# Kernel tuning notes

Hardware: AMD Instinct MI355X
Metric: run time of the kernel (lower is better)

## Reference

```python
import jax, jax.numpy as jnp
import numpy as np

NUM_EMBEDDINGS = 8192
EMBEDDING_DIM = 256
PROJECTION_DIM = 128


def setup_inputs() -> dict:
    key = jax.random.key(0)
    k_x, k_cb, k_w, k_b = jax.random.split(key, 4)
    x = jax.random.normal(k_x, (16, 1024, EMBEDDING_DIM), dtype=jnp.float32)
    codebook = jax.random.normal(k_cb, (NUM_EMBEDDINGS, EMBEDDING_DIM), dtype=jnp.float32)
    proj_w = jax.random.normal(k_w, (EMBEDDING_DIM, PROJECTION_DIM), dtype=jnp.float32) / np.sqrt(EMBEDDING_DIM)
    proj_b = jax.random.normal(k_b, (PROJECTION_DIM,), dtype=jnp.float32) * 0.01
    return {"x": x, "codebook": codebook, "proj_w": proj_w, "proj_b": proj_b}


def reference(x, codebook, proj_w, proj_b):
    # Flatten tokens: [N, D]
    x_flat = x.reshape(-1, EMBEDDING_DIM)
    # Project tokens and codebook into the distance space: [N, P], [K, P]
    x_proj = x_flat @ proj_w + proj_b
    cb_proj = codebook @ proj_w + proj_b
    # Squared euclidean distances via expansion: [N, K]
    distances = (
        jnp.sum(x_proj ** 2, axis=1, keepdims=True)
        - 2.0 * (x_proj @ cb_proj.T)
        + jnp.sum(cb_proj ** 2, axis=1)
    )
    idx = jnp.argmin(distances, axis=1)
    discrete = jax.nn.one_hot(idx, NUM_EMBEDDINGS, dtype=x.dtype)  # [N, K]
    # One-hot matmul lookup (disguised gather): [N, D]
    quantized = (discrete @ codebook).reshape(x.shape)
    return (discrete, quantized)
```

## Files before the change

kernel.cpp:

```cpp
#include <hip/hip_runtime.h>
#include <math.h>

#define D 256
#define P 128
#define K 8192
#define NTOK 16384
#define NROWS (NTOK + K)
#define CAPC 64
#define MARGIN 3.0f
#define FLT_BIG 3.402823466e+38f

typedef __attribute__((ext_vector_type(8))) short bf16x8;
typedef __attribute__((ext_vector_type(4))) float f32x4;
typedef __attribute__((ext_vector_type(8))) unsigned short u16x8;

__device__ __forceinline__ unsigned short f32_to_bf16_rne(float f) {
    unsigned int u = __float_as_uint(f);
    u = (u + 0x7fffu + ((u >> 16) & 1u)) >> 16;
    return (unsigned short)u;
}

__global__ __launch_bounds__(256) void proj_kernel(
    const float* __restrict__ x, const float* __restrict__ cb,
    const float* __restrict__ w, const float* __restrict__ bias,
    float* __restrict__ xproj, float* __restrict__ cproj,
    float* __restrict__ xnorm, float* __restrict__ cnorm,
    unsigned short* __restrict__ xh, unsigned short* __restrict__ chs,
    int* __restrict__ cnt, int* __restrict__ gmin)
{
    __shared__ float As[16][D];
    const int tid = threadIdx.x;
    const int row0 = blockIdx.x * 16;

    {
        int g = blockIdx.x * 256 + tid;
        if (g < NTOK) { cnt[g] = 0; gmin[g] = 0x7F7FFFFF; }
    }

    for (int i = tid; i < 16 * (D / 4); i += 256) {
        int r = i / (D / 4);
        int c4 = i % (D / 4);
        int gr = row0 + r;
        const float* src = (gr < NTOK) ? (x + (size_t)gr * D)
                                       : (cb + (size_t)(gr - NTOK) * D);
        float4 v = ((const float4*)src)[c4];
        ((float4*)&As[r][0])[c4] = v;
    }
    __syncthreads();

    const int r = tid >> 4;
    const int c0 = (tid & 15) * 8;

    float acc[8];
#pragma unroll
    for (int j = 0; j < 8; j++) acc[j] = 0.f;

    for (int d = 0; d < D; d += 4) {
        float4 a4 = *(const float4*)&As[r][d];
#pragma unroll
        for (int dd = 0; dd < 4; dd++) {
            float av = (dd == 0) ? a4.x : (dd == 1) ? a4.y : (dd == 2) ? a4.z : a4.w;
            float4 w0 = *(const float4*)&w[(size_t)(d + dd) * P + c0];
            float4 w1 = *(const float4*)&w[(size_t)(d + dd) * P + c0 + 4];
            acc[0] = fmaf(av, w0.x, acc[0]);
            acc[1] = fmaf(av, w0.y, acc[1]);
            acc[2] = fmaf(av, w0.z, acc[2]);
            acc[3] = fmaf(av, w0.w, acc[3]);
            acc[4] = fmaf(av, w1.x, acc[4]);
            acc[5] = fmaf(av, w1.y, acc[5]);
            acc[6] = fmaf(av, w1.z, acc[6]);
            acc[7] = fmaf(av, w1.w, acc[7]);
        }
    }

    float out[8];
    float nrm = 0.f;
    u16x8 hv;
#pragma unroll
    for (int j = 0; j < 8; j++) {
        out[j] = acc[j] + bias[c0 + j];
        nrm = fmaf(out[j], out[j], nrm);
        hv[j] = f32_to_bf16_rne(out[j]);
    }

    const int gr = row0 + r;
    float4 o0; o0.x = out[0]; o0.y = out[1]; o0.z = out[2]; o0.w = out[3];
    float4 o1; o1.x = out[4]; o1.y = out[5]; o1.z = out[6]; o1.w = out[7];
    if (gr < NTOK) {
        float* dst = xproj + (size_t)gr * P;
        *(float4*)&dst[c0] = o0;
        *(float4*)&dst[c0 + 4] = o1;
        *(u16x8*)(xh + (size_t)gr * P + c0) = hv;
    } else {
        int row = gr - NTOK;
        float* dst = cproj + (size_t)row * P;
        *(float4*)&dst[c0] = o0;
        *(float4*)&dst[c0 + 4] = o1;
        int t64 = row >> 6, rg = (row >> 4) & 3, rl = row & 15;
        int ks = c0 >> 5, q = (c0 >> 3) & 3;
        size_t atom = ((size_t)(t64 * 16 + rg * 4 + ks) * 4 + q) * 16 + rl;
        *(u16x8*)(chs + atom * 8) = hv;
    }

#pragma unroll
    for (int off = 1; off < 16; off <<= 1)
        nrm += __shfl_xor(nrm, off, 16);
    if ((tid & 15) == 0) {
        if (gr < NTOK) xnorm[gr] = nrm;
        else           cnorm[gr - NTOK] = nrm;
    }
}

__global__ __launch_bounds__(256, 3) void minzero_kernel(
    const unsigned short* __restrict__ xh, const unsigned short* __restrict__ chs,
    const float* __restrict__ xnorm, const float* __restrict__ cnorm,
    int* __restrict__ gmin, float* __restrict__ discrete)
{
    const int tid = threadIdx.x;
    const int tok0 = blockIdx.x * 128;
    const int kbase = blockIdx.y * 2048;
    const int flat = blockIdx.y * gridDim.x + blockIdx.x;

    const int wave = tid >> 6;
    const int lane = tid & 63;
    const int quad = lane >> 4;
    const int l15 = lane & 15;
    const int trow = tok0 + wave * 32;

    f32x4* zbase = (f32x4*)discrete + (size_t)flat * 65536;
    const f32x4 zv = (f32x4)(0.f);

    bf16x8 afrag[2][4];
#pragma unroll
    for (int mi = 0; mi < 2; mi++)
#pragma unroll
        for (int ks = 0; ks < 4; ks++)
            afrag[mi][ks] = *(const bf16x8*)(
                xh + (size_t)(trow + mi * 16 + l15) * P + ks * 32 + quad * 8);

    float xnv[2][4];
#pragma unroll
    for (int mi = 0; mi < 2; mi++)
#pragma unroll
        for (int r = 0; r < 4; r++)
            xnv[mi][r] = xnorm[trow + mi * 16 + quad * 4 + r];

    float rmin[2][4];
#pragma unroll
    for (int mi = 0; mi < 2; mi++)
#pragma unroll
        for (int r = 0; r < 4; r++) rmin[mi][r] = FLT_BIG;

    for (int ct = 0; ct < 32; ct++) {
        const int kt = kbase + ct * 64;
        const int t64 = kt >> 6;

#pragma unroll
        for (int s = 0; s < 8; s++)
            zbase[(size_t)ct * 2048 + s * 256 + tid] = zv;

        f32x4 acc[2][4];
#pragma unroll
        for (int mi = 0; mi < 2; mi++)
#pragma unroll
            for (int nj = 0; nj < 4; nj++) acc[mi][nj] = (f32x4)(0.f);

#pragma unroll
        for (int ks = 0; ks < 4; ks++) {
            const bf16x8* base = (const bf16x8*)(chs) + (size_t)(t64 * 16 + ks) * 64 + lane;
            bf16x8 b0 = base[0 * 4 * 64];
            bf16x8 b1 = base[1 * 4 * 64];
            bf16x8 b2 = base[2 * 4 * 64];
            bf16x8 b3 = base[3 * 4 * 64];
            acc[0][0] = __builtin_amdgcn_mfma_f32_16x16x32_bf16(afrag[0][ks], b0, acc[0][0], 0, 0, 0);
            acc[0][1] = __builtin_amdgcn_mfma_f32_16x16x32_bf16(afrag[0][ks], b1, acc[0][1], 0, 0, 0);
            acc[0][2] = __builtin_amdgcn_mfma_f32_16x16x32_bf16(afrag[0][ks], b2, acc[0][2], 0, 0, 0);
            acc[0][3] = __builtin_amdgcn_mfma_f32_16x16x32_bf16(afrag[0][ks], b3, acc[0][3], 0, 0, 0);
            acc[1][0] = __builtin_amdgcn_mfma_f32_16x16x32_bf16(afrag[1][ks], b0, acc[1][0], 0, 0, 0);
            acc[1][1] = __builtin_amdgcn_mfma_f32_16x16x32_bf16(afrag[1][ks], b1, acc[1][1], 0, 0, 0);
            acc[1][2] = __builtin_amdgcn_mfma_f32_16x16x32_bf16(afrag[1][ks], b2, acc[1][2], 0, 0, 0);
            acc[1][3] = __builtin_amdgcn_mfma_f32_16x16x32_bf16(afrag[1][ks], b3, acc[1][3], 0, 0, 0);
        }

        float cn[4];
#pragma unroll
        for (int nj = 0; nj < 4; nj++) cn[nj] = cnorm[kt + nj * 16 + l15];

#pragma unroll
        for (int mi = 0; mi < 2; mi++)
#pragma unroll
            for (int r = 0; r < 4; r++)
#pragma unroll
                for (int nj = 0; nj < 4; nj++) {
                    float dd = (xnv[mi][r] - 2.0f * acc[mi][nj][r]) + cn[nj];
                    rmin[mi][r] = fminf(rmin[mi][r], dd);
                }
    }

#pragma unroll
    for (int mi = 0; mi < 2; mi++)
#pragma unroll
        for (int r = 0; r < 4; r++) {
            float m = rmin[mi][r];
#pragma unroll
            for (int off = 1; off < 16; off <<= 1)
                m = fminf(m, __shfl_xor(m, off));
            if (l15 == 0)
                atomicMin(&gmin[trow + mi * 16 + quad * 4 + r], __float_as_int(m));
        }
}

__global__ __launch_bounds__(256, 3) void collect_kernel(
    const unsigned short* __restrict__ xh, const unsigned short* __restrict__ chs,
    const float* __restrict__ xnorm, const float* __restrict__ cnorm,
    const int* __restrict__ gmin,
    int* __restrict__ cnt, int* __restrict__ cand)
{
    const int tid = threadIdx.x;
    const int tok0 = blockIdx.x * 128;
    const int kbase = blockIdx.y * 2048;

    const int wave = tid >> 6;
    const int lane = tid & 63;
    const int quad = lane >> 4;
    const int l15 = lane & 15;
    const int trow = tok0 + wave * 32;

    bf16x8 afrag[2][4];
#pragma unroll
    for (int mi = 0; mi < 2; mi++)
#pragma unroll
        for (int ks = 0; ks < 4; ks++)
            afrag[mi][ks] = *(const bf16x8*)(
                xh + (size_t)(trow + mi * 16 + l15) * P + ks * 32 + quad * 8);

    float xnv[2][4], thr[2][4];
#pragma unroll
    for (int mi = 0; mi < 2; mi++)
#pragma unroll
        for (int r = 0; r < 4; r++) {
            int t = trow + mi * 16 + quad * 4 + r;
            xnv[mi][r] = xnorm[t];
            thr[mi][r] = __int_as_float(gmin[t]) + MARGIN;
        }

    for (int ct = 0; ct < 32; ct++) {
        const int kt = kbase + ct * 64;
        const int t64 = kt >> 6;

        f32x4 acc[2][4];
#pragma unroll
        for (int mi = 0; mi < 2; mi++)
#pragma unroll
            for (int nj = 0; nj < 4; nj++) acc[mi][nj] = (f32x4)(0.f);

#pragma unroll
        for (int ks = 0; ks < 4; ks++) {
            const bf16x8* base = (const bf16x8*)(chs) + (size_t)(t64 * 16 + ks) * 64 + lane;
            bf16x8 b0 = base[0 * 4 * 64];
            bf16x8 b1 = base[1 * 4 * 64];
            bf16x8 b2 = base[2 * 4 * 64];
            bf16x8 b3 = base[3 * 4 * 64];
            acc[0][0] = __builtin_amdgcn_mfma_f32_16x16x32_bf16(afrag[0][ks], b0, acc[0][0], 0, 0, 0);
            acc[0][1] = __builtin_amdgcn_mfma_f32_16x16x32_bf16(afrag[0][ks], b1, acc[0][1], 0, 0, 0);
            acc[0][2] = __builtin_amdgcn_mfma_f32_16x16x32_bf16(afrag[0][ks], b2, acc[0][2], 0, 0, 0);
            acc[0][3] = __builtin_amdgcn_mfma_f32_16x16x32_bf16(afrag[0][ks], b3, acc[0][3], 0, 0, 0);
            acc[1][0] = __builtin_amdgcn_mfma_f32_16x16x32_bf16(afrag[1][ks], b0, acc[1][0], 0, 0, 0);
            acc[1][1] = __builtin_amdgcn_mfma_f32_16x16x32_bf16(afrag[1][ks], b1, acc[1][1], 0, 0, 0);
            acc[1][2] = __builtin_amdgcn_mfma_f32_16x16x32_bf16(afrag[1][ks], b2, acc[1][2], 0, 0, 0);
            acc[1][3] = __builtin_amdgcn_mfma_f32_16x16x32_bf16(afrag[1][ks], b3, acc[1][3], 0, 0, 0);
        }

        float cn[4];
#pragma unroll
        for (int nj = 0; nj < 4; nj++) cn[nj] = cnorm[kt + nj * 16 + l15];

#pragma unroll
        for (int mi = 0; mi < 2; mi++)
#pragma unroll
            for (int r = 0; r < 4; r++) {
                const int tok = trow + mi * 16 + quad * 4 + r;
#pragma unroll
                for (int nj = 0; nj < 4; nj++) {
                    float dd = (xnv[mi][r] - 2.0f * acc[mi][nj][r]) + cn[nj];
                    if (dd <= thr[mi][r]) {
                        int pos = atomicAdd(&cnt[tok], 1);
                        if (pos < CAPC) cand[(size_t)tok * CAPC + pos] = kt + nj * 16 + l15;
                    }
                }
            }
    }
}

__global__ __launch_bounds__(256) void rescorefinal_kernel(
    const float* __restrict__ xproj, const float* __restrict__ cproj,
    const float* __restrict__ xnorm, const float* __restrict__ cnorm,
    const int* __restrict__ cnt, const int* __restrict__ cand,
    const float* __restrict__ cb,
    float* __restrict__ discrete, float* __restrict__ quant)
{
    __shared__ int sidx[64];
    const int tid = threadIdx.x;
    const int lane = tid & 63;
    const int wave = tid >> 6;
    const int tok0 = blockIdx.x * 64;

    for (int i = 0; i < 16; i++) {
        const int t = tok0 + wave * 16 + i;
        int n = cnt[t];
        if (n > CAPC) n = CAPC;
        const float xn = xnorm[t];
        const float* xr = xproj + (size_t)t * P;

        unsigned long long pack = 0xFFFFFFFFFFFFFFFFull;
        for (int j = lane; j < n; j += 64) {
            int k = cand[(size_t)t * CAPC + j];
            const float* cr = cproj + (size_t)k * P;
            float s = 0.f;
#pragma unroll 8
            for (int p = 0; p < P; p += 4) {
                float4 a = *(const float4*)&xr[p];
                float4 b = *(const float4*)&cr[p];
                s = fmaf(a.x, b.x, s);
                s = fmaf(a.y, b.y, s);
                s = fmaf(a.z, b.z, s);
                s = fmaf(a.w, b.w, s);
            }
            float dist = (xn - 2.0f * s) + cnorm[k];
            unsigned long long pk =
                ((unsigned long long)__float_as_uint(dist) << 32) |
                (unsigned long long)(unsigned)k;
            if (pk < pack) pack = pk;
        }
#pragma unroll
        for (int off = 1; off < 64; off <<= 1) {
            unsigned long long o = __shfl_xor((long long)pack, off);
            if (o < pack) pack = o;
        }
        if (lane == 0) {
            int bi = (int)(pack & 0xFFFFFFFFull);
            if (bi >= 0 && bi < K) {
                sidx[wave * 16 + i] = bi;
                discrete[(size_t)t * K + bi] = 1.0f;
            } else sidx[wave * 16 + i] = 0;
        }
    }
    __syncthreads();

    for (int i = tid; i < 64 * (D / 4); i += 256) {
        int t = i >> 6;
        int c4 = i & 63;
        int bi = sidx[t];
        float4 v = ((const float4*)(cb + (size_t)bi * D))[c4];
        ((float4*)(quant + (size_t)(tok0 + t) * D))[c4] = v;
    }
}

extern "C" void kernel_launch(void* const* d_in, const int* in_sizes, int n_in,
                              void* d_out, int out_size, void* d_ws, size_t ws_size,
                              hipStream_t stream) {
    const float* x    = (const float*)d_in[0];
    const float* cb   = (const float*)d_in[1];
    const float* w    = (const float*)d_in[2];
    const float* bias = (const float*)d_in[3];

    float* out = (float*)d_out;
    float* discrete = out;
    float* quant = out + (size_t)NTOK * K;

    char* ws = (char*)d_ws;
    size_t off = 0;
    float* xproj = (float*)(ws + off); off += (size_t)NTOK * P * 4;
    float* cproj = (float*)(ws + off); off += (size_t)K * P * 4;
    float* xnorm = (float*)(ws + off); off += (size_t)NTOK * 4;
    float* cnorm = (float*)(ws + off); off += (size_t)K * 4;
    unsigned short* xh  = (unsigned short*)(ws + off); off += (size_t)NTOK * P * 2;
    unsigned short* chs = (unsigned short*)(ws + off); off += (size_t)K * P * 2;
    int* cnt  = (int*)(ws + off); off += (size_t)NTOK * 4;
    int* cand = (int*)(ws + off); off += (size_t)NTOK * CAPC * 4;
    int* gmin = (int*)(ws + off); off += (size_t)NTOK * 4;

    proj_kernel<<<dim3(NROWS / 16), dim3(256), 0, stream>>>(
        x, cb, w, bias, xproj, cproj, xnorm, cnorm, xh, chs, cnt, gmin);

    minzero_kernel<<<dim3(NTOK / 128, 4), dim3(256), 0, stream>>>(
        xh, chs, xnorm, cnorm, gmin, discrete);

    collect_kernel<<<dim3(NTOK / 128, 4), dim3(256), 0, stream>>>(
        xh, chs, xnorm, cnorm, gmin, cnt, cand);

    rescorefinal_kernel<<<dim3(NTOK / 64), dim3(256), 0, stream>>>(
        xproj, cproj, xnorm, cnorm, cnt, cand, cb, discrete, quant);
}
```

Baseline: 869.2 us.

## Fuse min-finding and candidate collection into a single streaming pass

Merges the two bf16 MFMA passes (global min then threshold collection) into one kernel. Each block keeps a running per-row minimum and collects candidates within a margin of it, and the rescore kernel falls back to a full scan of all codes when a token overflows its candidate cap. This removes a full second distance GEMM and the gmin atomics. The cost is that early tiles use a looser running threshold, which produces more candidates and more overflow fallbacks to an expensive full rescore.

```diff
diff --git a/kernel.cpp b/kernel.cpp
--- a/kernel.cpp
+++ b/kernel.cpp
@@ -26,7 +26,7 @@
     float* __restrict__ xproj, float* __restrict__ cproj,
     float* __restrict__ xnorm, float* __restrict__ cnorm,
     unsigned short* __restrict__ xh, unsigned short* __restrict__ chs,
-    int* __restrict__ cnt, int* __restrict__ gmin)
+    int* __restrict__ cnt)
 {
     __shared__ float As[16][D];
     const int tid = threadIdx.x;
@@ -34,7 +34,7 @@
 
     {
         int g = blockIdx.x * 256 + tid;
-        if (g < NTOK) { cnt[g] = 0; gmin[g] = 0x7F7FFFFF; }
+        if (g < NTOK) cnt[g] = 0;
     }
 
     for (int i = tid; i < 16 * (D / 4); i += 256) {
@@ -111,10 +111,10 @@
     }
 }
 
-__global__ __launch_bounds__(256, 3) void minzero_kernel(
+__global__ __launch_bounds__(256, 3) void minzero_collect_kernel(
     const unsigned short* __restrict__ xh, const unsigned short* __restrict__ chs,
     const float* __restrict__ xnorm, const float* __restrict__ cnorm,
-    int* __restrict__ gmin, float* __restrict__ discrete)
+    int* __restrict__ cnt, int* __restrict__ cand, float* __restrict__ discrete)
 {
     const int tid = threadIdx.x;
     const int tok0 = blockIdx.x * 128;
@@ -186,109 +186,64 @@
 #pragma unroll
         for (int nj = 0; nj < 4; nj++) cn[nj] = cnorm[kt + nj * 16 + l15];
 
-#pragma unroll
-        for (int mi = 0; mi < 2; mi++)
-#pragma unroll
-            for (int r = 0; r < 4; r++)
-#pragma unroll
-                for (int nj = 0; nj < 4; nj++) {
-                    float dd = (xnv[mi][r] - 2.0f * acc[mi][nj][r]) + cn[nj];
-                    rmin[mi][r] = fminf(rmin[mi][r], dd);
-                }
-    }
-
-#pragma unroll
-    for (int mi = 0; mi < 2; mi++)
-#pragma unroll
-        for (int r = 0; r < 4; r++) {
-            float m = rmin[mi][r];
-#pragma unroll
-            for (int off = 1; off < 16; off <<= 1)
-                m = fminf(m, __shfl_xor(m, off));
-            if (l15 == 0)
-                atomicMin(&gmin[trow + mi * 16 + quad * 4 + r], __float_as_int(m));
-        }
-}
-
-__global__ __launch_bounds__(256, 3) void collect_kernel(
-    const unsigned short* __restrict__ xh, const unsigned short* __restrict__ chs,
-    const float* __restrict__ xnorm, const float* __restrict__ cnorm,
-    const int* __restrict__ gmin,
-    int* __restrict__ cnt, int* __restrict__ cand)
-{
-    const int tid = threadIdx.x;
-    const int tok0 = blockIdx.x * 128;
-    const int kbase = blockIdx.y * 2048;
-
-    const int wave = tid >> 6;
-    const int lane = tid & 63;
-    const int quad = lane >> 4;
-    const int l15 = lane & 15;
-    const int trow = tok0 + wave * 32;
-
-    bf16x8 afrag[2][4];
-#pragma unroll
-    for (int mi = 0; mi < 2; mi++)
-#pragma unroll
-        for (int ks = 0; ks < 4; ks++)
-            afrag[mi][ks] = *(const bf16x8*)(
-                xh + (size_t)(trow + mi * 16 + l15) * P + ks * 32 + quad * 8);
-
-    float xnv[2][4], thr[2][4];
-#pragma unroll
-    for (int mi = 0; mi < 2; mi++)
-#pragma unroll
-        for (int r = 0; r < 4; r++) {
-            int t = trow + mi * 16 + quad * 4 + r;
-            xnv[mi][r] = xnorm[t];
-            thr[mi][r] = __int_as_float(gmin[t]) + MARGIN;
-        }
-
-    for (int ct = 0; ct < 32; ct++) {
-        const int kt = kbase + ct * 64;
-        const int t64 = kt >> 6;
-
-        f32x4 acc[2][4];
-#pragma unroll
-        for (int mi = 0; mi < 2; mi++)
-#pragma unroll
-            for (int nj = 0; nj < 4; nj++) acc[mi][nj] = (f32x4)(0.f);
-
-#pragma unroll
-        for (int ks = 0; ks < 4; ks++) {
-            const bf16x8* base = (const bf16x8*)(chs) + (size_t)(t64 * 16 + ks) * 64 + lane;
-            bf16x8 b0 = base[0 * 4 * 64];
-            bf16x8 b1 = base[1 * 4 * 64];
-            bf16x8 b2 = base[2 * 4 * 64];
-            bf16x8 b3 = base[3 * 4 * 64];
-            acc[0][0] = __builtin_amdgcn_mfma_f32_16x16x32_bf16(afrag[0][ks], b0, acc[0][0], 0, 0, 0);
-            acc[0][1] = __builtin_amdgcn_mfma_f32_16x16x32_bf16(afrag[0][ks], b1, acc[0][1], 0, 0, 0);
-            acc[0][2] = __builtin_amdgcn_mfma_f32_16x16x32_bf16(afrag[0][ks], b2, acc[0][2], 0, 0, 0);
-            acc[0][3] = __builtin_amdgcn_mfma_f32_16x16x32_bf16(afrag[0][ks], b3, acc[0][3], 0, 0, 0);
-            acc[1][0] = __builtin_amdgcn_mfma_f32_16x16x32_bf16(afrag[1][ks], b0, acc[1][0], 0, 0, 0);
-            acc[1][1] = __builtin_amdgcn_mfma_f32_16x16x32_bf16(afrag[1][ks], b1, acc[1][1], 0, 0, 0);
-            acc[1][2] = __builtin_amdgcn_mfma_f32_16x16x32_bf16(afrag[1][ks], b2, acc[1][2], 0, 0, 0);
-            acc[1][3] = __builtin_amdgcn_mfma_f32_16x16x32_bf16(afrag[1][ks], b3, acc[1][3], 0, 0, 0);
-        }
-
-        float cn[4];
-#pragma unroll
-        for (int nj = 0; nj < 4; nj++) cn[nj] = cnorm[kt + nj * 16 + l15];
-
-#pragma unroll
-        for (int mi = 0; mi < 2; mi++)
-#pragma unroll
-            for (int r = 0; r < 4; r++) {
-                const int tok = trow + mi * 16 + quad * 4 + r;
-#pragma unroll
-                for (int nj = 0; nj < 4; nj++) {
-                    float dd = (xnv[mi][r] - 2.0f * acc[mi][nj][r]) + cn[nj];
-                    if (dd <= thr[mi][r]) {
-                        int pos = atomicAdd(&cnt[tok], 1);
-                        if (pos < CAPC) cand[(size_t)tok * CAPC + pos] = kt + nj * 16 + l15;
+        if (ct == 0) {
+#pragma unroll
+            for (int mi = 0; mi < 2; mi++)
+#pragma unroll
+                for (int r = 0; r < 4; r++) {
+                    float rm = rmin[mi][r];
+#pragma unroll
+                    for (int nj = 0; nj < 4; nj++) {
+                        float dd = (xnv[mi][r] - 2.0f * acc[mi][nj][r]) + cn[nj];
+                        rm = fminf(rm, dd);
+                    }
+#pragma unroll
+                    for (int off = 1; off < 16; off <<= 1)
+                        rm = fminf(rm, __shfl_xor(rm, off));
+                    rmin[mi][r] = rm;
+                    const float thr = rm + MARGIN;
+                    const int tok = trow + mi * 16 + quad * 4 + r;
+#pragma unroll
+                    for (int nj = 0; nj < 4; nj++) {
+                        float dd = (xnv[mi][r] - 2.0f * acc[mi][nj][r]) + cn[nj];
+                        if (dd <= thr) {
+                            int pos = atomicAdd(&cnt[tok], 1);
+                            if (pos < CAPC) cand[(size_t)tok * CAPC + pos] = kt + nj * 16 + l15;
+                        }
                     }
                 }
+        } else {
+#pragma unroll
+            for (int mi = 0; mi < 2; mi++)
+#pragma unroll
+                for (int r = 0; r < 4; r++) {
+                    float rm = rmin[mi][r];
+                    const float thr = rm + MARGIN;
+                    const int tok = trow + mi * 16 + quad * 4 + r;
+#pragma unroll
+                    for (int nj = 0; nj < 4; nj++) {
+                        float dd = (xnv[mi][r] - 2.0f * acc[mi][nj][r]) + cn[nj];
+                        rm = fminf(rm, dd);
+                        if (dd <= thr) {
+                            int pos = atomicAdd(&cnt[tok], 1);
+                            if (pos < CAPC) cand[(size_t)tok * CAPC + pos] = kt + nj * 16 + l15;
+                        }
+                    }
+                    rmin[mi][r] = rm;
+                }
+            if (ct & 1) {
+#pragma unroll
+                for (int mi = 0; mi < 2; mi++)
+#pragma unroll
+                    for (int r = 0; r < 4; r++) {
+                        float m = rmin[mi][r];
+#pragma unroll
+                        for (int off = 1; off < 16; off <<= 1)
+                            m = fminf(m, __shfl_xor(m, off));
+                        rmin[mi][r] = m;
+                    }
             }
+        }
     }
 }
 
@@ -307,14 +262,15 @@
 
     for (int i = 0; i < 16; i++) {
         const int t = tok0 + wave * 16 + i;
-        int n = cnt[t];
-        if (n > CAPC) n = CAPC;
+        const int n = cnt[t];
+        const bool full = (n > CAPC);
+        const int lim = full ? K : n;
         const float xn = xnorm[t];
         const float* xr = xproj + (size_t)t * P;
 
         unsigned long long pack = 0xFFFFFFFFFFFFFFFFull;
-        for (int j = lane; j < n; j += 64) {
-            int k = cand[(size_t)t * CAPC + j];
+        for (int j = lane; j < lim; j += 64) {
+            const int k = full ? j : cand[(size_t)t * CAPC + j];
             const float* cr = cproj + (size_t)k * P;
             float s = 0.f;
 #pragma unroll 8
@@ -378,16 +334,12 @@
     unsigned short* chs = (unsigned short*)(ws + off); off += (size_t)K * P * 2;
     int* cnt  = (int*)(ws + off); off += (size_t)NTOK * 4;
     int* cand = (int*)(ws + off); off += (size_t)NTOK * CAPC * 4;
-    int* gmin = (int*)(ws + off); off += (size_t)NTOK * 4;
 
     proj_kernel<<<dim3(NROWS / 16), dim3(256), 0, stream>>>(
-        x, cb, w, bias, xproj, cproj, xnorm, cnorm, xh, chs, cnt, gmin);
-
-    minzero_kernel<<<dim3(NTOK / 128, 4), dim3(256), 0, stream>>>(
-        xh, chs, xnorm, cnorm, gmin, discrete);
-
-    collect_kernel<<<dim3(NTOK / 128, 4), dim3(256), 0, stream>>>(
-        xh, chs, xnorm, cnorm, gmin, cnt, cand);
+        x, cb, w, bias, xproj, cproj, xnorm, cnorm, xh, chs, cnt);
+
+    minzero_collect_kernel<<<dim3(NTOK / 128, 4), dim3(256), 0, stream>>>(
+        xh, chs, xnorm, cnorm, cnt, cand, discrete);
 
     rescorefinal_kernel<<<dim3(NTOK / 64), dim3(256), 0, stream>>>(
         xproj, cproj, xnorm, cnorm, cnt, cand, cb, discrete, quant);
```

Result: faster. 844.2 us (median of 2 runs) (-2.9%).
